# Kernel optimization log

Hardware: AMD Instinct MI355X
Metric: run time of the kernel (lower is better)

The kernel has to match this reference:

```python
import jax, jax.numpy as jnp
import numpy as np

SAMPLE_RATE = 16000
N_TRANSIENTS = 20
TRANSIENT_SAMPLES = 1600  # int(0.1 s * 16000 Hz)
BATCH = 64
MAX_TRANSIENTS = 256
AUDIO_LEN = 160000  # 10 s @ 16 kHz


def setup_inputs() -> dict:
    key = jax.random.key(0)
    k1, k2, k3, k4 = jax.random.split(key, 4)
    # timings in seconds, sorted per batch (as in generate_random_transients)
    transient_timings = jnp.sort(
        jax.random.uniform(k1, (BATCH, MAX_TRANSIENTS), dtype=jnp.float32) * 9.0, axis=1)
    transient_ids = jax.random.randint(k2, (BATCH, MAX_TRANSIENTS), 0, N_TRANSIENTS)
    transient_gains = 0.1 + 0.9 * jax.random.uniform(k3, (BATCH, MAX_TRANSIENTS), dtype=jnp.float32)
    transient_templates = jax.random.normal(k4, (N_TRANSIENTS, TRANSIENT_SAMPLES), dtype=jnp.float32)
    return {
        "transient_timings": transient_timings,
        "transient_ids": transient_ids,
        "transient_gains": transient_gains,
        "transient_templates": transient_templates,
        "audio_length": AUDIO_LEN,
    }


def reference(transient_timings, transient_ids, transient_gains, transient_templates, audio_length):
    n_tr, L = transient_templates.shape
    # start sample of each transient (timings are non-negative, so floor == int())
    t_sample = jnp.floor(transient_timings * SAMPLE_RATE).astype(jnp.int32)  # [B, T]
    # skip conditions from the original loop: gain <= 0, id >= n_transients, start >= audio_length
    valid = (transient_gains > 0) & (transient_ids < n_tr) & (t_sample < audio_length)
    # gather templates: [B, T, L]
    tmpl = transient_templates[jnp.clip(transient_ids, 0, n_tr - 1)]
    vals = tmpl * (transient_gains * valid.astype(transient_gains.dtype))[..., None]
    # destination positions: [B, T, L]; positions >= audio_length are dropped (truncation)
    pos = t_sample[..., None] + jnp.arange(L, dtype=jnp.int32)

    def scatter_one(p, v):
        # p, v: [T, L] -> scatter-add into [audio_length]
        return jnp.zeros((audio_length,), v.dtype).at[p.reshape(-1)].add(
            v.reshape(-1), mode='drop')

    return jax.vmap(scatter_one)(pos, vals)  # [B, audio_length]
```

## Files before the change

kernel.cpp:

```cpp
#include <hip/hip_runtime.h>


constexpr int SR    = 16000;
constexpr int TL    = 1600;
constexpr int MAXT  = 256;
constexpr int CHUNK = 1024;

__global__ __launch_bounds__(256)
void transient_gather(const float* __restrict__ timings,
                      const int*   __restrict__ ids,
                      const float* __restrict__ gains,
                      const float* __restrict__ templates,
                      float*       __restrict__ out,
                      int T, int n_tr, int A, int bpb)
{
    __shared__ int   s_ts[MAXT];
    __shared__ float s_g [MAXT];
    __shared__ int   s_id[MAXT];

    const int b     = blockIdx.x / bpb;
    const int chunk = (blockIdx.x - b * bpb) * CHUNK;

    const float* bt = timings + (size_t)b * T;
    const float* bg = gains   + (size_t)b * T;
    const int*   bi = ids     + (size_t)b * T;

    for (int j = threadIdx.x; j < T; j += blockDim.x) {
        const float tm = bt[j];
        const int   ts = (int)floorf(tm * (float)SR);
        float g  = bg[j];
        int   id = bi[j];
        const bool ok = (g > 0.0f) & (id >= 0) & (id < n_tr) & (ts < A);
        s_ts[j] = ts;
        s_g [j] = ok ? g : 0.0f;
        s_id[j] = ok ? id : 0;
    }
    __syncthreads();

    const int p0 = chunk + (int)threadIdx.x * 4;
    float acc[4] = {0.f, 0.f, 0.f, 0.f};

    const int chunk_end = chunk + CHUNK;
    int lo = 0, hi = T;
    const int key = chunk - TL + 1;
    while (lo < hi) { const int m = (lo + hi) >> 1; if (s_ts[m] < key) lo = m + 1; else hi = m; }

    for (int j = lo; j < T; ++j) {
        const int ts = s_ts[j];
        if (ts >= chunk_end) break;
        const float g = s_g[j];
        const float* __restrict__ row = templates + (size_t)s_id[j] * TL;
        const int off = p0 - ts;
        if (off >= 0 && off + 3 < TL) {
#pragma unroll
            for (int k = 0; k < 4; ++k) acc[k] += g * row[off + k];
        } else {
#pragma unroll
            for (int k = 0; k < 4; ++k) {
                const int o = off + k;
                if (o >= 0 && o < TL) acc[k] += g * row[o];
            }
        }
    }

    float* op = out + (size_t)b * A + p0;
    if (p0 + 3 < A && ((((size_t)op) & 15) == 0)) {
        *reinterpret_cast<float4*>(op) = make_float4(acc[0], acc[1], acc[2], acc[3]);
    } else {
#pragma unroll
        for (int k = 0; k < 4; ++k) if (p0 + k < A) op[k] = acc[k];
    }
}

extern "C" void kernel_launch(void* const* d_in, const int* in_sizes, int n_in,
                              void* d_out, int out_size, void* d_ws, size_t ws_size,
                              hipStream_t stream) {
    const float* timings   = (const float*)d_in[0];
    const int*   ids       = (const int*)  d_in[1];
    const float* gains     = (const float*)d_in[2];
    const float* templates = (const float*)d_in[3];
    float*       out       = (float*)d_out;

    const int T    = MAXT;
    const int B    = in_sizes[0] / T;
    const int n_tr = in_sizes[3] / TL;
    const int A    = out_size / B;
    const int bpb  = (A + CHUNK - 1) / CHUNK;

    dim3 grid(B * bpb), block(256);
    transient_gather<<<grid, block, 0, stream>>>(timings, ids, gains, templates, out,
                                                 T, n_tr, A, bpb);
}
```

Measured before the change: 26.68 us.

## Process four sub-chunks per block and pack transient metadata into int2

New measurement: 33.93 us. 27.2% more time.

```diff
diff --git a/kernel.cpp b/kernel.cpp
--- a/kernel.cpp
+++ b/kernel.cpp
@@ -4,7 +4,9 @@
 constexpr int SR    = 16000;
 constexpr int TL    = 1600;
 constexpr int MAXT  = 256;
-constexpr int CHUNK = 1024;
+constexpr int SUB   = 1024;
+constexpr int NSUB  = 4;
+constexpr int SUPER = SUB * NSUB;
 
 __global__ __launch_bounds__(256)
 void transient_gather(const float* __restrict__ timings,
@@ -12,14 +14,12 @@
                       const float* __restrict__ gains,
                       const float* __restrict__ templates,
                       float*       __restrict__ out,
-                      int T, int n_tr, int A, int bpb)
+                      int T, int n_tr, int A)
 {
-    __shared__ int   s_ts[MAXT];
-    __shared__ float s_g [MAXT];
-    __shared__ int   s_id[MAXT];
+    __shared__ int2 s_m[MAXT];
 
-    const int b     = blockIdx.x / bpb;
-    const int chunk = (blockIdx.x - b * bpb) * CHUNK;
+    const int b     = blockIdx.y;
+    const int super = blockIdx.x * SUPER;
 
     const float* bt = timings + (size_t)b * T;
     const float* bg = gains   + (size_t)b * T;
@@ -28,47 +28,62 @@
     for (int j = threadIdx.x; j < T; j += blockDim.x) {
         const float tm = bt[j];
         const int   ts = (int)floorf(tm * (float)SR);
-        float g  = bg[j];
-        int   id = bi[j];
-        const bool ok = (g > 0.0f) & (id >= 0) & (id < n_tr) & (ts < A);
-        s_ts[j] = ts;
-        s_g [j] = ok ? g : 0.0f;
-        s_id[j] = ok ? id : 0;
+        const float g  = bg[j];
+        const int   id = bi[j];
+        const bool ok  = (g > 0.0f) & (id < n_tr) & (ts < A);
+        const int  idc = min(max(id, 0), n_tr - 1);
+        const int  tsc = min(ts, A);
+        s_m[j] = make_int2((tsc << 8) | idc, ok ? __float_as_int(g) : 0);
     }
     __syncthreads();
 
-    const int p0 = chunk + (int)threadIdx.x * 4;
-    float acc[4] = {0.f, 0.f, 0.f, 0.f};
+    const int p0 = super + (int)threadIdx.x * 4;
+    float4 acc[NSUB];
+#pragma unroll
+    for (int k = 0; k < NSUB; ++k) acc[k] = make_float4(0.f, 0.f, 0.f, 0.f);
 
-    const int chunk_end = chunk + CHUNK;
     int lo = 0, hi = T;
-    const int key = chunk - TL + 1;
-    while (lo < hi) { const int m = (lo + hi) >> 1; if (s_ts[m] < key) lo = m + 1; else hi = m; }
+    const int keyp = (super - TL + 1) << 8;
+    while (lo < hi) { const int m = (lo + hi) >> 1; if (s_m[m].x < keyp) lo = m + 1; else hi = m; }
 
+    const int endp = (super + SUPER) << 8;
     for (int j = lo; j < T; ++j) {
-        const int ts = s_ts[j];
-        if (ts >= chunk_end) break;
-        const float g = s_g[j];
-        const float* __restrict__ row = templates + (size_t)s_id[j] * TL;
-        const int off = p0 - ts;
-        if (off >= 0 && off + 3 < TL) {
+        const int2 mj = s_m[j];
+        if (mj.x >= endp) break;
+        const int   ts = mj.x >> 8;
+        const float g  = __int_as_float(mj.y);
+        const float* __restrict__ row = templates + (size_t)(mj.x & 255) * TL;
 #pragma unroll
-            for (int k = 0; k < 4; ++k) acc[k] += g * row[off + k];
-        } else {
-#pragma unroll
-            for (int k = 0; k < 4; ++k) {
-                const int o = off + k;
-                if (o >= 0 && o < TL) acc[k] += g * row[o];
+        for (int k = 0; k < NSUB; ++k) {
+            const int sub0 = super + k * SUB;
+            if (ts >= sub0 + SUB || ts + TL <= sub0) continue;
+            const int off = p0 + k * SUB - ts;
+            if (off >= 0 && off + 3 < TL) {
+                acc[k].x += g * row[off];
+                acc[k].y += g * row[off + 1];
+                acc[k].z += g * row[off + 2];
+                acc[k].w += g * row[off + 3];
+            } else if (off + 3 >= 0 && off < TL) {
+                if (off     >= 0 && off     < TL) acc[k].x += g * row[off];
+                if (off + 1 >= 0 && off + 1 < TL) acc[k].y += g * row[off + 1];
+                if (off + 2 >= 0 && off + 2 < TL) acc[k].z += g * row[off + 2];
+                if (off + 3 >= 0 && off + 3 < TL) acc[k].w += g * row[off + 3];
             }
         }
     }
 
-    float* op = out + (size_t)b * A + p0;
-    if (p0 + 3 < A && ((((size_t)op) & 15) == 0)) {
-        *reinterpret_cast<float4*>(op) = make_float4(acc[0], acc[1], acc[2], acc[3]);
-    } else {
 #pragma unroll
-        for (int k = 0; k < 4; ++k) if (p0 + k < A) op[k] = acc[k];
+    for (int k = 0; k < NSUB; ++k) {
+        const int p = p0 + k * SUB;
+        float* op = out + (size_t)b * A + p;
+        if (p + 3 < A) {
+            *reinterpret_cast<float4*>(op) = acc[k];
+        } else {
+            if (p     < A) op[0] = acc[k].x;
+            if (p + 1 < A) op[1] = acc[k].y;
+            if (p + 2 < A) op[2] = acc[k].z;
+            if (p + 3 < A) op[3] = acc[k].w;
+        }
     }
 }
 
@@ -85,9 +100,8 @@
     const int B    = in_sizes[0] / T;
     const int n_tr = in_sizes[3] / TL;
     const int A    = out_size / B;
-    const int bpb  = (A + CHUNK - 1) / CHUNK;
 
-    dim3 grid(B * bpb), block(256);
+    dim3 grid((A + SUPER - 1) / SUPER, B), block(256);
     transient_gather<<<grid, block, 0, stream>>>(timings, ids, gains, templates, out,
-                                                 T, n_tr, A, bpb);
+                                                 T, n_tr, A);
 }
```

## Split transient gather into per-batch prep kernel and lean gather kernel

Applied to the files above, without the earlier changes.

After: 30.54 us. +14.5%, slower.

```diff
diff --git a/kernel.cpp b/kernel.cpp
--- a/kernel.cpp
+++ b/kernel.cpp
@@ -7,68 +7,132 @@
 constexpr int CHUNK = 1024;
 
 __global__ __launch_bounds__(256)
-void transient_gather(const float* __restrict__ timings,
-                      const int*   __restrict__ ids,
-                      const float* __restrict__ gains,
-                      const float* __restrict__ templates,
-                      float*       __restrict__ out,
-                      int T, int n_tr, int A, int bpb)
+void prep(const float* __restrict__ timings, const int* __restrict__ ids,
+          const float* __restrict__ gains,
+          int2* __restrict__ meta,
+          int2* __restrict__ ranges,
+          int T, int n_tr, int A, int nchunk)
 {
-    __shared__ int   s_ts[MAXT];
-    __shared__ float s_g [MAXT];
-    __shared__ int   s_id[MAXT];
-
-    const int b     = blockIdx.x / bpb;
-    const int chunk = (blockIdx.x - b * bpb) * CHUNK;
-
-    const float* bt = timings + (size_t)b * T;
-    const float* bg = gains   + (size_t)b * T;
-    const int*   bi = ids     + (size_t)b * T;
+    __shared__ int s_ts[MAXT];
+    const int b = blockIdx.x;
 
     for (int j = threadIdx.x; j < T; j += blockDim.x) {
-        const float tm = bt[j];
+        const float tm = timings[(size_t)b * T + j];
         const int   ts = (int)floorf(tm * (float)SR);
-        float g  = bg[j];
-        int   id = bi[j];
-        const bool ok = (g > 0.0f) & (id >= 0) & (id < n_tr) & (ts < A);
-        s_ts[j] = ts;
-        s_g [j] = ok ? g : 0.0f;
-        s_id[j] = ok ? id : 0;
+        const float g  = gains[(size_t)b * T + j];
+        const int   id = ids[(size_t)b * T + j];
+        const bool ok  = (g > 0.0f) & (id < n_tr) & (ts < A);
+        const int idc  = min(max(id, 0), n_tr - 1);
+        const int tsc  = min(max(ts, 0), A);
+        s_ts[j] = tsc;
+        meta[(size_t)b * T + j] = make_int2((tsc << 8) | idc, ok ? __float_as_int(g) : 0);
     }
     __syncthreads();
 
-    const int p0 = chunk + (int)threadIdx.x * 4;
-    float acc[4] = {0.f, 0.f, 0.f, 0.f};
+    for (int c = threadIdx.x; c < nchunk; c += blockDim.x) {
+        const int chunk = c * CHUNK;
+        const int key_lo = max(0, chunk - TL + 1);
+        const int key_hi = chunk + CHUNK;
+        int lo = 0, hi = T;
+        while (lo < hi) { const int m = (lo + hi) >> 1; if (s_ts[m] < key_lo) lo = m + 1; else hi = m; }
+        int lo2 = lo, hi2 = T;
+        while (lo2 < hi2) { const int m = (lo2 + hi2) >> 1; if (s_ts[m] < key_hi) lo2 = m + 1; else hi2 = m; }
+        ranges[(size_t)b * nchunk + c] = make_int2(lo, lo2);
+    }
+}
 
-    const int chunk_end = chunk + CHUNK;
-    int lo = 0, hi = T;
-    const int key = chunk - TL + 1;
-    while (lo < hi) { const int m = (lo + hi) >> 1; if (s_ts[m] < key) lo = m + 1; else hi = m; }
+__global__ __launch_bounds__(256)
+void gather(const int2* __restrict__ meta, const int2* __restrict__ ranges,
+            const float* __restrict__ templates, float* __restrict__ out,
+            int T, int A, int nchunk)
+{
+    const int b     = blockIdx.y;
+    const int c     = blockIdx.x;
+    const int chunk = c * CHUNK;
+    const int2 r    = ranges[(size_t)b * nchunk + c];
+    const int p0    = chunk + (int)threadIdx.x * 4;
 
-    for (int j = lo; j < T; ++j) {
-        const int ts = s_ts[j];
-        if (ts >= chunk_end) break;
-        const float g = s_g[j];
-        const float* __restrict__ row = templates + (size_t)s_id[j] * TL;
+    float4 acc = make_float4(0.f, 0.f, 0.f, 0.f);
+    const int2* __restrict__ mb = meta + (size_t)b * T;
+
+    for (int j = r.x; j < r.y; ++j) {
+        const int2  m  = mb[j];
+        const int   ts = m.x >> 8;
+        const float g  = __int_as_float(m.y);
+        const float* __restrict__ row = templates + (size_t)(m.x & 255) * TL;
         const int off = p0 - ts;
         if (off >= 0 && off + 3 < TL) {
-#pragma unroll
-            for (int k = 0; k < 4; ++k) acc[k] += g * row[off + k];
-        } else {
-#pragma unroll
-            for (int k = 0; k < 4; ++k) {
-                const int o = off + k;
-                if (o >= 0 && o < TL) acc[k] += g * row[o];
-            }
+            acc.x += g * row[off];
+            acc.y += g * row[off + 1];
+            acc.z += g * row[off + 2];
+            acc.w += g * row[off + 3];
+        } else if (off + 3 >= 0 && off < TL) {
+            if (off     >= 0 && off     < TL) acc.x += g * row[off];
+            if (off + 1 >= 0 && off + 1 < TL) acc.y += g * row[off + 1];
+            if (off + 2 >= 0 && off + 2 < TL) acc.z += g * row[off + 2];
+            if (off + 3 >= 0 && off + 3 < TL) acc.w += g * row[off + 3];
         }
     }
 
     float* op = out + (size_t)b * A + p0;
-    if (p0 + 3 < A && ((((size_t)op) & 15) == 0)) {
-        *reinterpret_cast<float4*>(op) = make_float4(acc[0], acc[1], acc[2], acc[3]);
+    if (p0 + 3 < A) {
+        *reinterpret_cast<float4*>(op) = acc;
     } else {
-#pragma unroll
-        for (int k = 0; k < 4; ++k) if (p0 + k < A) op[k] = acc[k];
+        if (p0     < A) op[0] = acc.x;
+        if (p0 + 1 < A) op[1] = acc.y;
+        if (p0 + 2 < A) op[2] = acc.z;
+        if (p0 + 3 < A) op[3] = acc.w;
+    }
+}
+
+__global__ __launch_bounds__(256)
+void gather_fb(const float* __restrict__ timings, const int* __restrict__ ids,
+               const float* __restrict__ gains, const float* __restrict__ templates,
+               float* __restrict__ out, int T, int n_tr, int A)
+{
+    __shared__ int2 s_m[MAXT];
+    const int b = blockIdx.y;
+    const int chunk = blockIdx.x * CHUNK;
+    for (int j = threadIdx.x; j < T; j += blockDim.x) {
+        const float tm = timings[(size_t)b * T + j];
+        const int ts = (int)floorf(tm * (float)SR);
+        const float g = gains[(size_t)b * T + j];
+        const int id = ids[(size_t)b * T + j];
+        const bool ok = (g > 0.0f) & (id < n_tr) & (ts < A);
+        s_m[j] = make_int2((min(max(ts, 0), A) << 8) | min(max(id, 0), n_tr - 1),
+                           ok ? __float_as_int(g) : 0);
+    }
+    __syncthreads();
+    const int p0 = chunk + (int)threadIdx.x * 4;
+    float4 acc = make_float4(0.f, 0.f, 0.f, 0.f);
+    int lo = 0, hi = T;
+    const int keyp = max(0, chunk - TL + 1) << 8;
+    while (lo < hi) { const int m = (lo + hi) >> 1; if (s_m[m].x < keyp) lo = m + 1; else hi = m; }
+    const int endp = (chunk + CHUNK) << 8;
+    for (int j = lo; j < T; ++j) {
+        const int2 m = s_m[j];
+        if (m.x >= endp) break;
+        const int ts = m.x >> 8;
+        const float g = __int_as_float(m.y);
+        const float* __restrict__ row = templates + (size_t)(m.x & 255) * TL;
+        const int off = p0 - ts;
+        if (off >= 0 && off + 3 < TL) {
+            acc.x += g * row[off]; acc.y += g * row[off + 1];
+            acc.z += g * row[off + 2]; acc.w += g * row[off + 3];
+        } else if (off + 3 >= 0 && off < TL) {
+            if (off     >= 0 && off     < TL) acc.x += g * row[off];
+            if (off + 1 >= 0 && off + 1 < TL) acc.y += g * row[off + 1];
+            if (off + 2 >= 0 && off + 2 < TL) acc.z += g * row[off + 2];
+            if (off + 3 >= 0 && off + 3 < TL) acc.w += g * row[off + 3];
+        }
+    }
+    float* op = out + (size_t)b * A + p0;
+    if (p0 + 3 < A) { *reinterpret_cast<float4*>(op) = acc; }
+    else {
+        if (p0 < A) op[0] = acc.x;
+        if (p0 + 1 < A) op[1] = acc.y;
+        if (p0 + 2 < A) op[2] = acc.z;
+        if (p0 + 3 < A) op[3] = acc.w;
     }
 }
 
@@ -81,13 +145,22 @@
     const float* templates = (const float*)d_in[3];
     float*       out       = (float*)d_out;
 
-    const int T    = MAXT;
-    const int B    = in_sizes[0] / T;
-    const int n_tr = in_sizes[3] / TL;
-    const int A    = out_size / B;
-    const int bpb  = (A + CHUNK - 1) / CHUNK;
+    const int T      = MAXT;
+    const int B      = in_sizes[0] / T;
+    const int n_tr   = in_sizes[3] / TL;
+    const int A      = out_size / B;
+    const int nchunk = (A + CHUNK - 1) / CHUNK;
 
-    dim3 grid(B * bpb), block(256);
-    transient_gather<<<grid, block, 0, stream>>>(timings, ids, gains, templates, out,
-                                                 T, n_tr, A, bpb);
+    const size_t need = (size_t)B * T * sizeof(int2) + (size_t)B * nchunk * sizeof(int2);
+    if (ws_size >= need) {
+        int2* meta   = (int2*)d_ws;
+        int2* rangesp = meta + (size_t)B * T;
+        prep<<<dim3(B), dim3(256), 0, stream>>>(timings, ids, gains, meta, rangesp,
+                                                T, n_tr, A, nchunk);
+        gather<<<dim3(nchunk, B), dim3(256), 0, stream>>>(meta, rangesp, templates, out,
+                                                          T, A, nchunk);
+    } else {
+        gather_fb<<<dim3(nchunk, B), dim3(256), 0, stream>>>(timings, ids, gains,
+                                                             templates, out, T, n_tr, A);
+    }
 }
```

## Pack transient metadata, use ballot masks for range, stride-interleave output elements

Applied to the files above, without the earlier changes.

Result: no change. 26.20 us (-1.8%).

```diff
diff --git a/kernel.cpp b/kernel.cpp
--- a/kernel.cpp
+++ b/kernel.cpp
@@ -4,71 +4,71 @@
 constexpr int SR    = 16000;
 constexpr int TL    = 1600;
 constexpr int MAXT  = 256;
+constexpr int NTHR  = 256;
 constexpr int CHUNK = 1024;
 
-__global__ __launch_bounds__(256)
+__global__ __launch_bounds__(NTHR)
 void transient_gather(const float* __restrict__ timings,
                       const int*   __restrict__ ids,
                       const float* __restrict__ gains,
                       const float* __restrict__ templates,
                       float*       __restrict__ out,
-                      int T, int n_tr, int A, int bpb)
+                      int T, int n_tr, int A)
 {
-    __shared__ int   s_ts[MAXT];
-    __shared__ float s_g [MAXT];
-    __shared__ int   s_id[MAXT];
+    __shared__ int2               s_m[MAXT];
+    __shared__ unsigned long long s_mask[NTHR / 64];
 
-    const int b     = blockIdx.x / bpb;
-    const int chunk = (blockIdx.x - b * bpb) * CHUNK;
+    const int b      = blockIdx.y;
+    const int chunk0 = blockIdx.x * CHUNK;
+    const int tid    = (int)threadIdx.x;
 
-    const float* bt = timings + (size_t)b * T;
-    const float* bg = gains   + (size_t)b * T;
-    const int*   bi = ids     + (size_t)b * T;
+    {
+        const float tm = timings[(size_t)b * T + tid];
+        const float g  = gains  [(size_t)b * T + tid];
+        const int   id = ids    [(size_t)b * T + tid];
+        const int   ts = (int)floorf(tm * (float)SR);
+        const bool ok  = (g > 0.0f) & (id < n_tr) & (ts < A);
+        const int tsc  = min(max(ts, 0), A);
+        const int idc  = min(max(id, 0), n_tr - 1);
+        s_m[tid] = make_int2((tsc << 8) | idc, ok ? __float_as_int(g) : 0);
 
-    for (int j = threadIdx.x; j < T; j += blockDim.x) {
-        const float tm = bt[j];
-        const int   ts = (int)floorf(tm * (float)SR);
-        float g  = bg[j];
-        int   id = bi[j];
-        const bool ok = (g > 0.0f) & (id >= 0) & (id < n_tr) & (ts < A);
-        s_ts[j] = ts;
-        s_g [j] = ok ? g : 0.0f;
-        s_id[j] = ok ? id : 0;
+        const bool ov = (tsc < chunk0 + CHUNK) && (tsc + TL > chunk0);
+        const unsigned long long m = __ballot(ov);
+        if ((tid & 63) == 0) s_mask[tid >> 6] = m;
     }
     __syncthreads();
 
-    const int p0 = chunk + (int)threadIdx.x * 4;
-    float acc[4] = {0.f, 0.f, 0.f, 0.f};
-
-    const int chunk_end = chunk + CHUNK;
-    int lo = 0, hi = T;
-    const int key = chunk - TL + 1;
-    while (lo < hi) { const int m = (lo + hi) >> 1; if (s_ts[m] < key) lo = m + 1; else hi = m; }
-
-    for (int j = lo; j < T; ++j) {
-        const int ts = s_ts[j];
-        if (ts >= chunk_end) break;
-        const float g = s_g[j];
-        const float* __restrict__ row = templates + (size_t)s_id[j] * TL;
-        const int off = p0 - ts;
-        if (off >= 0 && off + 3 < TL) {
+    int lo = T, hi = -1;
 #pragma unroll
-            for (int k = 0; k < 4; ++k) acc[k] += g * row[off + k];
-        } else {
-#pragma unroll
-            for (int k = 0; k < 4; ++k) {
-                const int o = off + k;
-                if (o >= 0 && o < TL) acc[k] += g * row[o];
-            }
+    for (int w = 0; w < NTHR / 64; ++w) {
+        const unsigned long long mw = s_mask[w];
+        if (mw) {
+            lo = min(lo, w * 64 + (int)__builtin_ctzll(mw));
+            hi = max(hi, w * 64 + 63 - (int)__builtin_clzll(mw));
         }
     }
 
-    float* op = out + (size_t)b * A + p0;
-    if (p0 + 3 < A && ((((size_t)op) & 15) == 0)) {
-        *reinterpret_cast<float4*>(op) = make_float4(acc[0], acc[1], acc[2], acc[3]);
-    } else {
+    float acc[4] = {0.f, 0.f, 0.f, 0.f};
+    const int off_base = chunk0 + tid;
+
+    for (int j = lo; j <= hi; ++j) {
+        const int2  m  = s_m[j];
+        const int   ts = m.x >> 8;
+        const float g  = __int_as_float(m.y);
+        const float* __restrict__ row = templates + (size_t)(m.x & 255) * TL;
+        const int off0 = off_base - ts;
 #pragma unroll
-        for (int k = 0; k < 4; ++k) if (p0 + k < A) op[k] = acc[k];
+        for (int k = 0; k < 4; ++k) {
+            const int o = off0 + k * NTHR;
+            if ((unsigned)o < (unsigned)TL)
+                acc[k] += g * row[o];
+        }
+    }
+
+    float* ob = out + (size_t)b * A + off_base;
+#pragma unroll
+    for (int k = 0; k < 4; ++k) {
+        if (off_base + k * NTHR < A) ob[k * NTHR] = acc[k];
     }
 }
 
@@ -85,9 +85,8 @@
     const int B    = in_sizes[0] / T;
     const int n_tr = in_sizes[3] / TL;
     const int A    = out_size / B;
-    const int bpb  = (A + CHUNK - 1) / CHUNK;
 
-    dim3 grid(B * bpb), block(256);
+    dim3 grid((A + CHUNK - 1) / CHUNK, B), block(NTHR);
     transient_gather<<<grid, block, 0, stream>>>(timings, ids, gains, templates, out,
-                                                 T, n_tr, A, bpb);
+                                                 T, n_tr, A);
 }
```
